# Optimization experiments

Measured on AMD Instinct MI355X. Metric: run time of the kernel, lower is better.

## Reference

```python
import jax, jax.numpy as jnp
import numpy as np
from jax import lax

K = 512   # codebook size (clusternumber)
D = 16    # feature dim = channels after conv4 (arch=2)

def conv2d_same(x, w, b):
    # x: (B,C,H,W), w: (O,I,3,3) -> same-padded stride-1 conv
    y = lax.conv_general_dilated(x, w, (1, 1), 'SAME',
                                 dimension_numbers=('NCHW', 'OIHW', 'NCHW'))
    return y + b[None, :, None, None]

def maxpool2(x):
    return lax.reduce_window(x, -jnp.inf, lax.max, (1, 1, 2, 2), (1, 1, 2, 2), 'VALID')

def setup_inputs() -> dict:
    key = jax.random.key(0)
    ks = jax.random.split(key, 16)
    s = 0.05
    return {
        'x':        jax.random.normal(ks[0], (64, 3, 64, 64), jnp.float32),
        'w1':       jax.random.normal(ks[1], (16, 3, 3, 3), jnp.float32) * s,
        'b1':       jnp.zeros((16,), jnp.float32),
        'w2':       jax.random.normal(ks[2], (16, 16, 3, 3), jnp.float32) * s,
        'b2':       jnp.zeros((16,), jnp.float32),
        'w3':       jax.random.normal(ks[3], (24, 16, 3, 3), jnp.float32) * s,
        'b3':       jnp.zeros((24,), jnp.float32),
        'w4':       jax.random.normal(ks[4], (16, 24, 3, 3), jnp.float32) * s,
        'b4':       jnp.zeros((16,), jnp.float32),
        'codebook': jax.random.normal(ks[5], (K, D), jnp.float32) * 0.1,
        'sigma':    jax.random.uniform(ks[6], (K,), jnp.float32, 0.05, 0.15),
        'l1_w':     jax.random.normal(ks[7], (20, K), jnp.float32) * (1.0 / np.sqrt(K)),
        'l1_b':     jnp.zeros((20,), jnp.float32),
        'l2_w':     jax.random.normal(ks[8], (10, 20), jnp.float32) * (1.0 / np.sqrt(20)),
        'l2_b':     jnp.zeros((10,), jnp.float32),
    }

def reference(x, w1, b1, w2, b2, w3, b3, w4, b4, codebook, sigma,
              l1_w, l1_b, l2_w, l2_b):
    # CNN trunk (arch=2, bofnumber=4): conv,conv,pool,conv,conv with relu
    h = jax.nn.relu(conv2d_same(x, w1, b1))
    h = jax.nn.relu(conv2d_same(h, w2, b2))
    h = maxpool2(h)
    h = jax.nn.relu(conv2d_same(h, w3, b3))
    h = jax.nn.relu(conv2d_same(h, w4, b4))
    B, C, H, W = h.shape
    f = h.reshape(B, C, H * W).transpose(0, 2, 1)          # (B, N, D)
    # squared euclidean distance via norm expansion (same math as
    # sum(|x - c|^2), avoids materializing (B,K,N,D))
    f2 = jnp.sum(f * f, axis=2)                            # (B, N)
    c2 = jnp.sum(codebook * codebook, axis=1)              # (K,)
    cross = jnp.einsum('bnd,kd->bkn', f, codebook)         # (B, K, N)
    dist = f2[:, None, :] + c2[None, :, None] - 2.0 * cross
    a = jnp.exp(-dist * sigma[None, :, None])              # RBF membership
    # F.normalize(p=1, dim=1) over the K codebook axis
    a = a / jnp.clip(jnp.sum(jnp.abs(a), axis=1, keepdims=True), 1e-12)
    pooled = jnp.mean(a, axis=2)                           # (B, K)
    z = jax.nn.relu(pooled @ l1_w.T + l1_b)
    return z @ l2_w.T + l2_b                               # (B, 10)
```

## Files before the change

### kernel.cpp

```cpp
#include <hip/hip_runtime.h>
#include <hip/hip_bf16.h>

#define KCB 512
#define DF  16
#define BATCH 64

__device__ __forceinline__ float bperm(int addr, float v) {
    return __int_as_float(__builtin_amdgcn_ds_bpermute(addr, __float_as_int(v)));
}

__global__ __launch_bounds__(256) void wtrans_kernel(
    const float* __restrict__ w1, const float* __restrict__ w2,
    const float* __restrict__ w3, const float* __restrict__ w4,
    float* __restrict__ wt1, float* __restrict__ wt2,
    float* __restrict__ wt3, float* __restrict__ wt4)
{
    int i = blockIdx.x * 256 + threadIdx.x;
    if (i < 432) {
        int o = i & 15, rest = i >> 4;
        int kx = rest % 3, ky = (rest / 3) % 3, c = rest / 9;
        wt1[i] = w1[((o * 3 + c) * 3 + ky) * 3 + kx];
        return;
    }
    i -= 432;
    if (i < 2304) {
        int o = i & 15, rest = i >> 4;
        int kx = rest % 3, ky = (rest / 3) % 3, c = rest / 9;
        wt2[i] = w2[((o * 16 + c) * 3 + ky) * 3 + kx];
        return;
    }
    i -= 2304;
    if (i < 3456) {
        int o = i % 24, rest = i / 24;
        int kx = rest % 3, ky = (rest / 3) % 3, c = rest / 9;
        wt3[i] = w3[((o * 16 + c) * 3 + ky) * 3 + kx];
        return;
    }
    i -= 3456;
    if (i < 3456) {
        int o = i & 15, rest = i >> 4;
        int kx = rest % 3, ky = (rest / 3) % 3, c = rest / 9;
        wt4[i] = w4[((o * 24 + c) * 3 + ky) * 3 + kx];
    }
}

template<int CIN, int COUT_T, int COUT_TOTAL>
__global__ __launch_bounds__(256) void conv_row64_kernel(
    const float* __restrict__ in, const float* __restrict__ wt,
    const float* __restrict__ bias, float* __restrict__ out)
{
    const int H = 64, W = 64;
    const int lane = threadIdx.x & 63;
    const int wv = threadIdx.x >> 6;
    const int y = blockIdx.x * 4 + wv;
    const int og = blockIdx.y * COUT_T;
    const int b = blockIdx.z;
    const int x = lane;
    const int xl = max(x - 1, 0);
    const int xr = min(x + 1, W - 1);

    float acc[COUT_T];
#pragma unroll
    for (int o = 0; o < COUT_T; ++o) acc[o] = bias[og + o];

#pragma unroll
    for (int c = 0; c < CIN; ++c) {
        const float* ip = in + ((size_t)(b * CIN + c) * H) * W;
#pragma unroll
        for (int ky = 0; ky < 3; ++ky) {
            int ry = y + ky - 1;
            int ryc = min(max(ry, 0), H - 1);
            const float* rp = ip + ryc * W;
            float tc = rp[x], tl = rp[xl], tr = rp[xr];
            bool ok = (ry == ryc);
            float vc = ok ? tc : 0.f;
            float vl = (ok && x > 0)     ? tl : 0.f;
            float vr = (ok && x < W - 1) ? tr : 0.f;
            const float* wp = wt + ((c * 3 + ky) * 3) * COUT_TOTAL + og;
#pragma unroll
            for (int o = 0; o < COUT_T; ++o) acc[o] = fmaf(vl, wp[o], acc[o]);
#pragma unroll
            for (int o = 0; o < COUT_T; ++o) acc[o] = fmaf(vc, wp[COUT_TOTAL + o], acc[o]);
#pragma unroll
            for (int o = 0; o < COUT_T; ++o) acc[o] = fmaf(vr, wp[2 * COUT_TOTAL + o], acc[o]);
        }
    }
#pragma unroll
    for (int o = 0; o < COUT_T; ++o)
        out[((b * COUT_TOTAL + og + o) * H + y) * W + x] = fmaxf(acc[o], 0.f);
}

__global__ __launch_bounds__(512) void conv2_split_kernel(
    const float* __restrict__ in, const float* __restrict__ wt,
    const float* __restrict__ bias, float* __restrict__ out)
{
    const int CIN = 16, H = 64, W = 64, WAVES = 8;
    __shared__ float s_acc[WAVES][64][34];
    const int t = threadIdx.x;
    const int lane = t & 63;
    const int wv = t >> 6;
    const int r = blockIdx.x;
    const int y0 = r * 2;
    const int b = blockIdx.y;
    const int x = lane;
    const int xl = max(x - 1, 0);
    const int xr = min(x + 1, W - 1);

    float acc0[16], acc1[16];
#pragma unroll
    for (int o = 0; o < 16; ++o) {
        float bz = (wv == 0) ? bias[o] : 0.f;
        acc0[o] = bz; acc1[o] = bz;
    }

#pragma unroll
    for (int ci = 0; ci < 2; ++ci) {
        const int c = wv * 2 + ci;
        const float* ip = in + ((size_t)(b * CIN + c) * H) * W;
        float v[4], vl[4], vr[4];
#pragma unroll
        for (int j = 0; j < 4; ++j) {
            int ry = y0 - 1 + j;
            int ryc = min(max(ry, 0), H - 1);
            const float* rp = ip + ryc * W;
            float tc = rp[x], tl = rp[xl], tr = rp[xr];
            bool ok = (ry == ryc);
            v[j]  = ok ? tc : 0.f;
            vl[j] = (ok && x > 0)     ? tl : 0.f;
            vr[j] = (ok && x < W - 1) ? tr : 0.f;
        }
#pragma unroll
        for (int ky = 0; ky < 3; ++ky) {
            const float* wp = wt + ((c * 3 + ky) * 3) * 16;
#pragma unroll
            for (int kx = 0; kx < 3; ++kx) {
                float a0 = (kx == 0) ? vl[ky]     : (kx == 1) ? v[ky]     : vr[ky];
                float a1 = (kx == 0) ? vl[ky + 1] : (kx == 1) ? v[ky + 1] : vr[ky + 1];
                const float* wq = wp + kx * 16;
#pragma unroll
                for (int o = 0; o < 16; ++o) {
                    float w = wq[o];
                    acc0[o] = fmaf(a0, w, acc0[o]);
                    acc1[o] = fmaf(a1, w, acc1[o]);
                }
            }
        }
    }
#pragma unroll
    for (int o = 0; o < 16; ++o) {
        s_acc[wv][x][2 * o]     = acc0[o];
        s_acc[wv][x][2 * o + 1] = acc1[o];
    }
    __syncthreads();

    float s00 = 0.f, s01 = 0.f, s10 = 0.f, s11 = 0.f;
#pragma unroll
    for (int w2 = 0; w2 < WAVES; ++w2) {
        float2 p0 = *(const float2*)&s_acc[w2][x][4 * wv];
        float2 p1 = *(const float2*)&s_acc[w2][x][4 * wv + 2];
        s00 += p0.x; s01 += p0.y; s10 += p1.x; s11 += p1.y;
    }
    float m0 = fmaxf(s00, s01);
    float m1 = fmaxf(s10, s11);
    m0 = fmaxf(m0, __shfl_xor(m0, 1));
    m1 = fmaxf(m1, __shfl_xor(m1, 1));
    m0 = fmaxf(m0, 0.f);
    m1 = fmaxf(m1, 0.f);
    if ((x & 1) == 0) {
        const int px = x >> 1;
        out[((b * 16 + 2 * wv) * 32 + r) * 32 + px]     = m0;
        out[((b * 16 + 2 * wv + 1) * 32 + r) * 32 + px] = m1;
    }
}

__global__ __launch_bounds__(512) void conv3_split_kernel(
    const float* __restrict__ in, const float* __restrict__ wt,
    const float* __restrict__ bias, float* __restrict__ out)
{
    const int CIN = 16, COUT = 24, H = 32, W = 32, WAVES = 8, CPW = 2;
    __shared__ float s_acc[WAVES][64][COUT + 1];
    const int t = threadIdx.x;
    const int lane = t & 63;
    const int wv = t >> 6;
    const int p = blockIdx.x;
    const int b = blockIdx.y;
    const int h = lane >> 5;
    const int x = lane & 31;
    const int y = p * 2 + h;
    const int xl = max(x - 1, 0);
    const int xr = min(x + 1, W - 1);

    float acc[COUT];
#pragma unroll
    for (int o = 0; o < COUT; ++o) acc[o] = (wv == 0) ? bias[o] : 0.f;

#pragma unroll
    for (int ci = 0; ci < CPW; ++ci) {
        const int c = wv * CPW + ci;
        const float* ip = in + ((size_t)(b * CIN + c) * H) * W;
        float v[3], vl[3], vr[3];
#pragma unroll
        for (int d = 0; d < 3; ++d) {
            int ry = y + d - 1;
            int ryc = min(max(ry, 0), H - 1);
            const float* rp = ip + ryc * W;
            float tc = rp[x], tl = rp[xl], tr = rp[xr];
            bool ok = (ry == ryc);
            v[d]  = ok ? tc : 0.f;
            vl[d] = (ok && x > 0)     ? tl : 0.f;
            vr[d] = (ok && x < W - 1) ? tr : 0.f;
        }
#pragma unroll
        for (int ky = 0; ky < 3; ++ky) {
#pragma unroll
            for (int kx = 0; kx < 3; ++kx) {
                float a = (kx == 0) ? vl[ky] : (kx == 1) ? v[ky] : vr[ky];
                const float* wq = wt + ((c * 3 + ky) * 3 + kx) * COUT;
#pragma unroll
                for (int o = 0; o < COUT; ++o)
                    acc[o] = fmaf(a, wq[o], acc[o]);
            }
        }
    }
#pragma unroll
    for (int o = 0; o < COUT; ++o) s_acc[wv][lane][o] = acc[o];
    __syncthreads();

    const int pl = t >> 3;
    const int ob = (t & 7) * 3;
    const int yy = p * 2 + (pl >> 5);
    const int xx = pl & 31;
#pragma unroll
    for (int k = 0; k < 3; ++k) {
        float s = 0.f;
#pragma unroll
        for (int w2 = 0; w2 < WAVES; ++w2) s += s_acc[w2][pl][ob + k];
        out[((b * COUT + ob + k) * H + yy) * W + xx] = fmaxf(s, 0.f);
    }
}

__global__ __launch_bounds__(512) void conv4_split_kernel(
    const float* __restrict__ in, const float* __restrict__ wt,
    const float* __restrict__ bias, float* __restrict__ ft,
    float* __restrict__ f2)
{
    const int CIN = 24, COUT = 16, H = 32, W = 32, WAVES = 8, CPW = 3;
    __shared__ float s_acc[WAVES][64][COUT + 1];
    const int t = threadIdx.x;
    const int lane = t & 63;
    const int wv = t >> 6;
    const int p = blockIdx.x;
    const int b = blockIdx.y;
    const int h = lane >> 5;
    const int x = lane & 31;
    const int y = p * 2 + h;
    const int xl = max(x - 1, 0);
    const int xr = min(x + 1, W - 1);

    float acc[COUT];
#pragma unroll
    for (int o = 0; o < COUT; ++o) acc[o] = (wv == 0) ? bias[o] : 0.f;

#pragma unroll
    for (int ci = 0; ci < CPW; ++ci) {
        const int c = wv * CPW + ci;
        const float* ip = in + ((size_t)(b * CIN + c) * H) * W;
        float v[3], vl[3], vr[3];
#pragma unroll
        for (int d = 0; d < 3; ++d) {
            int ry = y + d - 1;
            int ryc = min(max(ry, 0), H - 1);
            const float* rp = ip + ryc * W;
            float tc = rp[x], tl = rp[xl], tr = rp[xr];
            bool ok = (ry == ryc);
            v[d]  = ok ? tc : 0.f;
            vl[d] = (ok && x > 0)     ? tl : 0.f;
            vr[d] = (ok && x < W - 1) ? tr : 0.f;
        }
#pragma unroll
        for (int ky = 0; ky < 3; ++ky) {
#pragma unroll
            for (int kx = 0; kx < 3; ++kx) {
                float a = (kx == 0) ? vl[ky] : (kx == 1) ? v[ky] : vr[ky];
                const float* wq = wt + ((c * 3 + ky) * 3 + kx) * COUT;
#pragma unroll
                for (int o = 0; o < COUT; ++o)
                    acc[o] = fmaf(a, wq[o], acc[o]);
            }
        }
    }
#pragma unroll
    for (int o = 0; o < COUT; ++o) s_acc[wv][lane][o] = acc[o];
    __syncthreads();

    const int pl = t >> 3;
    const int o2 = (t & 7) * 2;
    float s0 = 0.f, s1 = 0.f;
#pragma unroll
    for (int w2 = 0; w2 < WAVES; ++w2) {
        s0 += s_acc[w2][pl][o2];
        s1 += s_acc[w2][pl][o2 + 1];
    }
    s0 = fmaxf(s0, 0.f);
    s1 = fmaxf(s1, 0.f);
    const size_t pix = (size_t)b * 1024 + (p * 2 + (pl >> 5)) * W + (pl & 31);
    *(float2*)(ft + pix * 16 + o2) = make_float2(s0, s1);
    float q = fmaf(s1, s1, s0 * s0);
    q += __shfl_xor(q, 1);
    q += __shfl_xor(q, 2);
    q += __shfl_xor(q, 4);
    if ((t & 7) == 0) f2[pix] = q;
}

__global__ __launch_bounds__(512) void bof_kernel(
    const float* __restrict__ ft, const float* __restrict__ f2,
    const float* __restrict__ codebook, const float* __restrict__ sigma,
    float* __restrict__ partial)
{
    const int J = 16;
    const int PIX = 64;
    const int b = blockIdx.y;
    const int chunk = blockIdx.x;
    const int t = threadIdx.x;
    const int lane = t & 63;
    const int w = t >> 6;

    __shared__ float s_e[KCB][J + 1];
    __shared__ float s_q[8][16];
    __shared__ float s_dinv[J];
    __shared__ float s_f2[PIX];

    const size_t base = (size_t)b * 1024 + chunk * PIX;
    if (t < PIX) s_f2[t] = f2[base + t];

    float cb[DF];
    {
        const float4* cq = (const float4*)(codebook + (size_t)t * DF);
        float4 a0 = cq[0], a1 = cq[1], a2 = cq[2], a3 = cq[3];
        cb[0]=a0.x; cb[1]=a0.y; cb[2]=a0.z; cb[3]=a0.w;
        cb[4]=a1.x; cb[5]=a1.y; cb[6]=a1.z; cb[7]=a1.w;
        cb[8]=a2.x; cb[9]=a2.y; cb[10]=a2.z; cb[11]=a2.w;
        cb[12]=a3.x; cb[13]=a3.y; cb[14]=a3.z; cb[15]=a3.w;
    }
    float c2 = 0.f;
#pragma unroll
    for (int d = 0; d < DF; ++d) c2 = fmaf(cb[d], cb[d], c2);
    const float sg = sigma[t];

    __syncthreads();

    float acc = 0.f;

    for (int jb = 0; jb < PIX / J; ++jb) {
        const int j0 = jb * J;
        float e[J];
#pragma unroll
        for (int jj = 0; jj < J; ++jj) {
            const float* fp = ft + (base + j0 + jj) * DF;
            float dot = 0.f;
#pragma unroll
            for (int d = 0; d < DF; ++d) dot = fmaf(fp[d], cb[d], dot);
            float f2c = s_f2[j0 + jj] + c2;
            float dist = fmaf(-2.f, dot, f2c);
            e[jj] = __expf(-dist * sg);
            s_e[t][jj] = e[jj];
        }
        __syncthreads();

        {
            const int c   = t & 15;
            const int seg = t >> 4;
            float ps = 0.f;
#pragma unroll
            for (int rr = 0; rr < 16; ++rr) ps += s_e[seg * 16 + rr][c];
            ps += __shfl_xor(ps, 16);
            ps += __shfl_xor(ps, 32);
            if (lane < 16) s_q[w][lane] = ps;
        }
        __syncthreads();

        if (t < J) {
            float dsum = 0.f;
#pragma unroll
            for (int i = 0; i < 8; ++i) dsum += s_q[i][t];
            s_dinv[t] = 1.f / fmaxf(dsum, 1e-12f);
        }
        __syncthreads();

#pragma unroll
        for (int jj = 0; jj < J; ++jj)
            acc = fmaf(e[jj], s_dinv[jj], acc);
    }
    partial[((size_t)b * 16 + chunk) * KCB + t] = acc;
}

__global__ __launch_bounds__(512) void tail_kernel(
    const float* __restrict__ partial,
    const float* __restrict__ l1w, const float* __restrict__ l1b,
    const float* __restrict__ l2w, const float* __restrict__ l2b,
    float* __restrict__ out)
{
    const int b = blockIdx.x;
    const int t = threadIdx.x;
    __shared__ float s_pool[KCB];
    __shared__ float s_z[20];

    float s = 0.f;
#pragma unroll
    for (int c = 0; c < 16; ++c)
        s += partial[((size_t)b * 16 + c) * KCB + t];
    s_pool[t] = s * (1.0f / 1024.0f);
    __syncthreads();

    if (t < 320) {
        const int row = t >> 4;
        const int l   = t & 15;
        float a = 0.f;
        const float* wr = l1w + (size_t)row * KCB;
#pragma unroll
        for (int m = 0; m < 32; ++m)
            a = fmaf(s_pool[l + 16 * m], wr[l + 16 * m], a);
#pragma unroll
        for (int off = 1; off < 16; off <<= 1)
            a += __shfl_xor(a, off);
        if (l == 0) s_z[row] = fmaxf(a + l1b[row], 0.f);
    }
    __syncthreads();

    if (t < 10) {
        float s2 = l2b[t];
#pragma unroll
        for (int j = 0; j < 20; ++j) s2 = fmaf(s_z[j], l2w[t * 20 + j], s2);
        out[b * 10 + t] = s2;
    }
}

extern "C" void kernel_launch(void* const* d_in, const int* in_sizes, int n_in,
                              void* d_out, int out_size, void* d_ws, size_t ws_size,
                              hipStream_t stream)
{
    const float* x        = (const float*)d_in[0];
    const float* w1       = (const float*)d_in[1];
    const float* b1       = (const float*)d_in[2];
    const float* w2       = (const float*)d_in[3];
    const float* b2       = (const float*)d_in[4];
    const float* w3       = (const float*)d_in[5];
    const float* b3       = (const float*)d_in[6];
    const float* w4       = (const float*)d_in[7];
    const float* b4       = (const float*)d_in[8];
    const float* codebook = (const float*)d_in[9];
    const float* sigma    = (const float*)d_in[10];
    const float* l1w      = (const float*)d_in[11];
    const float* l1b      = (const float*)d_in[12];
    const float* l2w      = (const float*)d_in[13];
    const float* l2b      = (const float*)d_in[14];
    float* out = (float*)d_out;

    float* ws = (float*)d_ws;
    const size_t N_WT1 = 432;
    const size_t N_WT2 = 2304;
    const size_t N_WT3 = 3456;
    const size_t N_WT4 = 3456;
    const size_t N_C1 = (size_t)BATCH * 16 * 64 * 64;
    const size_t N_P  = (size_t)BATCH * 16 * 32 * 32;
    const size_t N_C3 = (size_t)BATCH * 24 * 32 * 32;
    const size_t N_FT = (size_t)BATCH * 1024 * 16;
    const size_t N_F2 = (size_t)BATCH * 1024;
    const size_t N_PART = (size_t)BATCH * 16 * KCB;

    float* wt1  = ws;  ws += N_WT1;
    float* wt2  = ws;  ws += N_WT2;
    float* wt3  = ws;  ws += N_WT3;
    float* wt4  = ws;  ws += N_WT4;
    float* c1   = ws;  ws += N_C1;
    float* p    = ws;  ws += N_P;
    float* c3   = ws;  ws += N_C3;
    float* ft   = ws;  ws += N_FT;
    float* f2   = ws;  ws += N_F2;
    float* part = ws;  ws += N_PART;

    wtrans_kernel<<<38, 256, 0, stream>>>(w1, w2, w3, w4, wt1, wt2, wt3, wt4);
    conv_row64_kernel<3, 8, 16><<<dim3(16, 2, BATCH), 256, 0, stream>>>(x, wt1, b1, c1);
    conv2_split_kernel<<<dim3(32, BATCH), 512, 0, stream>>>(c1, wt2, b2, p);
    conv3_split_kernel<<<dim3(16, BATCH), 512, 0, stream>>>(p, wt3, b3, c3);
    conv4_split_kernel<<<dim3(16, BATCH), 512, 0, stream>>>(c3, wt4, b4, ft, f2);
    bof_kernel<<<dim3(16, BATCH), 512, 0, stream>>>(ft, f2, codebook, sigma, part);
    tail_kernel<<<BATCH, 512, 0, stream>>>(part, l1w, l1b, l2w, l2b, out);
}
```

Baseline: 144.2 us.

## Split conv2 work by row and channel group; compute BoF normalizers per wave

```diff
diff --git a/kernel.cpp b/kernel.cpp
--- a/kernel.cpp
+++ b/kernel.cpp
@@ -94,83 +94,74 @@
     const float* __restrict__ in, const float* __restrict__ wt,
     const float* __restrict__ bias, float* __restrict__ out)
 {
-    const int CIN = 16, H = 64, W = 64, WAVES = 8;
-    __shared__ float s_acc[WAVES][64][34];
+    const int CIN = 16, H = 64, W = 64;
+    __shared__ float s_acc[8][64][17];
     const int t = threadIdx.x;
     const int lane = t & 63;
     const int wv = t >> 6;
+    const int cg = wv >> 1;
+    const int row = wv & 1;
     const int r = blockIdx.x;
-    const int y0 = r * 2;
+    const int y = r * 2 + row;
     const int b = blockIdx.y;
     const int x = lane;
     const int xl = max(x - 1, 0);
     const int xr = min(x + 1, W - 1);
 
-    float acc0[16], acc1[16];
-#pragma unroll
-    for (int o = 0; o < 16; ++o) {
-        float bz = (wv == 0) ? bias[o] : 0.f;
-        acc0[o] = bz; acc1[o] = bz;
-    }
-
-#pragma unroll
-    for (int ci = 0; ci < 2; ++ci) {
-        const int c = wv * 2 + ci;
+    float acc[16];
+#pragma unroll
+    for (int o = 0; o < 16; ++o) acc[o] = (cg == 0) ? bias[o] : 0.f;
+
+#pragma unroll
+    for (int ci = 0; ci < 4; ++ci) {
+        const int c = cg * 4 + ci;
         const float* ip = in + ((size_t)(b * CIN + c) * H) * W;
-        float v[4], vl[4], vr[4];
-#pragma unroll
-        for (int j = 0; j < 4; ++j) {
-            int ry = y0 - 1 + j;
+        float v[3], vl[3], vr[3];
+#pragma unroll
+        for (int d = 0; d < 3; ++d) {
+            int ry = y + d - 1;
             int ryc = min(max(ry, 0), H - 1);
             const float* rp = ip + ryc * W;
             float tc = rp[x], tl = rp[xl], tr = rp[xr];
             bool ok = (ry == ryc);
-            v[j]  = ok ? tc : 0.f;
-            vl[j] = (ok && x > 0)     ? tl : 0.f;
-            vr[j] = (ok && x < W - 1) ? tr : 0.f;
+            v[d]  = ok ? tc : 0.f;
+            vl[d] = (ok && x > 0)     ? tl : 0.f;
+            vr[d] = (ok && x < W - 1) ? tr : 0.f;
         }
 #pragma unroll
         for (int ky = 0; ky < 3; ++ky) {
             const float* wp = wt + ((c * 3 + ky) * 3) * 16;
 #pragma unroll
             for (int kx = 0; kx < 3; ++kx) {
-                float a0 = (kx == 0) ? vl[ky]     : (kx == 1) ? v[ky]     : vr[ky];
-                float a1 = (kx == 0) ? vl[ky + 1] : (kx == 1) ? v[ky + 1] : vr[ky + 1];
+                float a = (kx == 0) ? vl[ky] : (kx == 1) ? v[ky] : vr[ky];
                 const float* wq = wp + kx * 16;
 #pragma unroll
-                for (int o = 0; o < 16; ++o) {
-                    float w = wq[o];
-                    acc0[o] = fmaf(a0, w, acc0[o]);
-                    acc1[o] = fmaf(a1, w, acc1[o]);
-                }
+                for (int o = 0; o < 16; ++o)
+                    acc[o] = fmaf(a, wq[o], acc[o]);
             }
         }
     }
 #pragma unroll
-    for (int o = 0; o < 16; ++o) {
-        s_acc[wv][x][2 * o]     = acc0[o];
-        s_acc[wv][x][2 * o + 1] = acc1[o];
-    }
-    __syncthreads();
-
-    float s00 = 0.f, s01 = 0.f, s10 = 0.f, s11 = 0.f;
-#pragma unroll
-    for (int w2 = 0; w2 < WAVES; ++w2) {
-        float2 p0 = *(const float2*)&s_acc[w2][x][4 * wv];
-        float2 p1 = *(const float2*)&s_acc[w2][x][4 * wv + 2];
-        s00 += p0.x; s01 += p0.y; s10 += p1.x; s11 += p1.y;
-    }
-    float m0 = fmaxf(s00, s01);
-    float m1 = fmaxf(s10, s11);
-    m0 = fmaxf(m0, __shfl_xor(m0, 1));
-    m1 = fmaxf(m1, __shfl_xor(m1, 1));
-    m0 = fmaxf(m0, 0.f);
-    m1 = fmaxf(m1, 0.f);
-    if ((x & 1) == 0) {
-        const int px = x >> 1;
-        out[((b * 16 + 2 * wv) * 32 + r) * 32 + px]     = m0;
-        out[((b * 16 + 2 * wv + 1) * 32 + r) * 32 + px] = m1;
-    }
+    for (int o = 0; o < 16; ++o) s_acc[wv][x][o] = acc[o];
+    __syncthreads();
+
+    const int o = t >> 5;
+    const int px = t & 31;
+    float m = -1e30f;
+#pragma unroll
+    for (int rw = 0; rw < 2; ++rw) {
+#pragma unroll
+        for (int dx = 0; dx < 2; ++dx) {
+            const int x2 = 2 * px + dx;
+            float s = 0.f;
+#pragma unroll
+            for (int cg2 = 0; cg2 < 4; ++cg2)
+                s += s_acc[cg2 * 2 + rw][x2][o];
+            m = fmaxf(m, s);
+        }
+    }
+    m = fmaxf(m, 0.f);
+    out[((b * 16 + o) * 32 + r) * 32 + px] = m;
 }
 
 __global__ __launch_bounds__(512) void conv3_split_kernel(
@@ -327,7 +318,6 @@
 
     __shared__ float s_e[KCB][J + 1];
     __shared__ float s_q[8][16];
-    __shared__ float s_dinv[J];
     __shared__ float s_f2[PIX];
 
     const size_t base = (size_t)b * 1024 + chunk * PIX;
@@ -379,17 +369,14 @@
         }
         __syncthreads();
 
-        if (t < J) {
-            float dsum = 0.f;
-#pragma unroll
-            for (int i = 0; i < 8; ++i) dsum += s_q[i][t];
-            s_dinv[t] = 1.f / fmaxf(dsum, 1e-12f);
-        }
-        __syncthreads();
+        float dsum = 0.f;
+#pragma unroll
+        for (int i = 0; i < 8; ++i) dsum += s_q[i][lane & 15];
+        float dinv = 1.f / fmaxf(dsum, 1e-12f);
 
 #pragma unroll
         for (int jj = 0; jj < J; ++jj)
-            acc = fmaf(e[jj], s_dinv[jj], acc);
+            acc = fmaf(e[jj], __shfl(dinv, jj), acc);
     }
     partial[((size_t)b * 16 + chunk) * KCB + t] = acc;
 }
```

Result: slower. 179.4 us (+24.4%).
